# Performance work log

Hardware: AMD Instinct MI355X
Metric: run time of the kernel (lower is better)

The kernel has to match this reference:

```python
import jax, jax.numpy as jnp
import numpy as np

B = 524288
NF, NH1, NH21, NH22, NCLS = 5, 128, 32, 32, 1


def setup_inputs() -> dict:
    key = jax.random.key(0)
    ks = jax.random.split(key, 12)
    s = 0.05
    return {
        "x": jax.random.normal(ks[0], (B, NF), dtype=jnp.float32),
        "mean": jnp.zeros((NF,), dtype=jnp.float32),
        "std": jnp.ones((NF,), dtype=jnp.float32),
        "W1": jax.random.normal(ks[1], (NH1, NF), dtype=jnp.float32) * s,
        "b1": jax.random.normal(ks[2], (NH1,), dtype=jnp.float32) * s,
        "W21": jax.random.normal(ks[3], (NH21, NH1), dtype=jnp.float32) * s,
        "b21": jax.random.normal(ks[4], (NH21,), dtype=jnp.float32) * s,
        "W22": jax.random.normal(ks[5], (NH22, NH1), dtype=jnp.float32) * s,
        "b22": jax.random.normal(ks[6], (NH22,), dtype=jnp.float32) * s,
        "W31": jax.random.normal(ks[7], (NCLS, NH21), dtype=jnp.float32) * s,
        "b31": jax.random.normal(ks[8], (NCLS,), dtype=jnp.float32) * s,
        "W32": jax.random.normal(ks[9], (NCLS, NH22), dtype=jnp.float32) * s,
        "b32": jax.random.normal(ks[10], (NCLS,), dtype=jnp.float32) * s,
    }


def reference(x, mean, std, W1, b1, W21, b21, W22, b22, W31, b31, W32, b32):
    # de-normalized state used to build the CBF inequality
    x0 = x * std + mean  # [B, 5]
    h1 = jax.nn.relu(x @ W1.T + b1)         # [B, 128]  (bn=False path)
    x21 = jax.nn.relu(h1 @ W21.T + b21)     # [B, 32]
    x22 = jax.nn.relu(h1 @ W22.T + b22)     # [B, 32]
    x31 = x21 @ W31.T + b31                 # [B, 1]  QP linear term p
    x32 = 4.0 * jax.nn.sigmoid(x22 @ W32.T + b32)  # [B, 1]  learned penalty
    # h for the single inequality 1.8*u <= h
    h = (x0[:, 1] - x0[:, 3])[:, None] + x32 * (x0[:, 0] - x0[:, 2] - 1.8 * x0[:, 3])[:, None]
    # Closed-form 1-D QP: min 0.5 u^2 + x31*u  s.t. 1.8 u <= h
    u_unc = -x31
    u = jnp.where(1.8 * u_unc <= h, u_unc, h / 1.8)  # [B, 1]
    return u
```

## Files before the change

### kernel.cpp

```cpp
#include <hip/hip_runtime.h>
#include <math.h>

typedef __attribute__((ext_vector_type(8))) short bf16x8;
typedef __attribute__((ext_vector_type(4))) float f32x4;
typedef __attribute__((ext_vector_type(4))) unsigned int u32x4;

#define BLK 256


__device__ __forceinline__ unsigned int rne_bf16_bits(float w) {
    unsigned int u = __builtin_bit_cast(unsigned int, w);
    u += 0x7fffu + ((u >> 16) & 1u);
    return u >> 16;
}

__global__ void setup_kernel(const float* __restrict__ W1, const float* __restrict__ b1,
                             const float* __restrict__ W21, const float* __restrict__ W22,
                             float* __restrict__ w1q, unsigned short* __restrict__ frg)
{
    int t = blockIdx.x * blockDim.x + threadIdx.x;
    if (t < 128) {
        int c  = t;
        int tt = c >> 5, r = c & 31, qq = r >> 3, j = r & 7;
        float* dst = w1q + ((tt * 8 + j) * 4 + qq) * 8;
        #pragma unroll
        for (int f = 0; f < 5; ++f) dst[f] = W1[c * 5 + f];
        dst[5] = b1[c];
        dst[6] = 0.0f;
        dst[7] = 0.0f;
    }
    for (int e = t; e < 16 * 64 * 8; e += 4096) {
        int F = e >> 9, l = (e >> 3) & 63, j = e & 7;
        int mat = F >> 3, nt = (F >> 2) & 1, kt = F & 3;
        int n = nt * 16 + (l & 15);
        int k = kt * 32 + (l >> 4) * 8 + j;
        const float* W = mat ? W22 : W21;
        frg[e] = (unsigned short)rne_bf16_bits(W[n * 128 + k]);
    }
}

__global__ __launch_bounds__(BLK, 3) void barriernet_kernel(
    const float* __restrict__ x,
    const float* __restrict__ mean, const float* __restrict__ stdv,
    const float* __restrict__ b21, const float* __restrict__ b22,
    const float* __restrict__ W31, const float* __restrict__ b31,
    const float* __restrict__ W32, const float* __restrict__ b32,
    const float* __restrict__ w1q, const u32x4* __restrict__ frg,
    float* __restrict__ out, int zero)
{
    __shared__ u32x4 ldsF[1024];
    __shared__ float ldsX[1280];

    const int tid = threadIdx.x;
    #pragma unroll
    for (int i = 0; i < 4; ++i) ldsF[tid + i * BLK] = frg[tid + i * BLK];
    const float* xblk = x + (size_t)blockIdx.x * 1280;
    #pragma unroll
    for (int i = 0; i < 5; ++i) ldsX[tid + i * BLK] = xblk[tid + i * BLK];

    const int lane = tid & 63;
    const int wave = tid >> 6;
    const int m    = lane & 15;
    const int q    = lane >> 4;

    float sm_s[5], sm_m[5];
    #pragma unroll
    for (int f = 0; f < 5; ++f) { sm_s[f] = stdv[f]; sm_m[f] = mean[f]; }

    const f32x4 b21a = *(const f32x4*)(b21 + q * 4);
    const f32x4 b21b = *(const f32x4*)(b21 + 16 + q * 4);
    const f32x4 b22a = *(const f32x4*)(b22 + q * 4);
    const f32x4 b22b = *(const f32x4*)(b22 + 16 + q * 4);
    const f32x4 w31a = *(const f32x4*)(W31 + q * 4);
    const f32x4 w31b = *(const f32x4*)(W31 + 16 + q * 4);
    const f32x4 w32a = *(const f32x4*)(W32 + q * 4);
    const f32x4 w32b = *(const f32x4*)(W32 + 16 + q * 4);
    const float b31s = b31[0], b32s = b32[0];

    __syncthreads();

    const size_t row0 = (size_t)blockIdx.x * 256;

    #pragma unroll 1
    for (int it = 0; it < 2; ++it) {
        const int tl0 = wave * 4 + it * 2;

        float xf[2][5];
        #pragma unroll
        for (int T = 0; T < 2; ++T)
            #pragma unroll
            for (int f = 0; f < 5; ++f)
                xf[T][f] = ldsX[((tl0 + T) * 16 + m) * 5 + f];

        const float* wz = w1q + it * zero;
        unsigned int au[2][4][4];
        #pragma unroll
        for (int t = 0; t < 4; ++t) {
            #pragma unroll
            for (int p = 0; p < 4; ++p) {
                const int g0 = ((t * 8 + p * 2) * 4 + q) * 8;
                const float4 a0 = *(const float4*)(wz + g0);
                const float4 a1 = *(const float4*)(wz + g0 + 4);
                const float4 c0 = *(const float4*)(wz + g0 + 32);
                const float4 c1 = *(const float4*)(wz + g0 + 36);
                #pragma unroll
                for (int T = 0; T < 2; ++T) {
                    float h0 = a1.y;
                    h0 = fmaf(xf[T][0], a0.x, h0);
                    h0 = fmaf(xf[T][1], a0.y, h0);
                    h0 = fmaf(xf[T][2], a0.z, h0);
                    h0 = fmaf(xf[T][3], a0.w, h0);
                    h0 = fmaf(xf[T][4], a1.x, h0);
                    h0 = fmaxf(h0, 0.0f);
                    float h1 = c1.y;
                    h1 = fmaf(xf[T][0], c0.x, h1);
                    h1 = fmaf(xf[T][1], c0.y, h1);
                    h1 = fmaf(xf[T][2], c0.z, h1);
                    h1 = fmaf(xf[T][3], c0.w, h1);
                    h1 = fmaf(xf[T][4], c1.x, h1);
                    h1 = fmaxf(h1, 0.0f);
                    au[T][t][p] = rne_bf16_bits(h0) | (rne_bf16_bits(h1) << 16);
                }
            }
        }

        f32x4 acc[2][4];
        #pragma unroll
        for (int T = 0; T < 2; ++T) {
            acc[T][0] = b21a; acc[T][1] = b21b;
            acc[T][2] = b22a; acc[T][3] = b22b;
        }
        const int fz = it * zero;
        #pragma unroll
        for (int kt = 0; kt < 4; ++kt) {
            bf16x8 bw[4];
            #pragma unroll
            for (int c = 0; c < 4; ++c) {
                const int F = (c >> 1) * 8 + (c & 1) * 4 + kt;
                bw[c] = __builtin_bit_cast(bf16x8, ldsF[F * 64 + lane + fz]);
            }
            #pragma unroll
            for (int T = 0; T < 2; ++T) {
                u32x4 t4 = { au[T][kt][0], au[T][kt][1], au[T][kt][2], au[T][kt][3] };
                bf16x8 a = __builtin_bit_cast(bf16x8, t4);
                #pragma unroll
                for (int c = 0; c < 4; ++c)
                    acc[T][c] = __builtin_amdgcn_mfma_f32_16x16x32_bf16(bw[c], a, acc[T][c], 0, 0, 0);
            }
        }

        #pragma unroll
        for (int T = 0; T < 2; ++T) {
            float s31 = 0.0f, s32 = 0.0f;
            #pragma unroll
            for (int r = 0; r < 4; ++r) {
                s31 = fmaf(fmaxf(acc[T][0][r], 0.0f), w31a[r], s31);
                s31 = fmaf(fmaxf(acc[T][1][r], 0.0f), w31b[r], s31);
                s32 = fmaf(fmaxf(acc[T][2][r], 0.0f), w32a[r], s32);
                s32 = fmaf(fmaxf(acc[T][3][r], 0.0f), w32b[r], s32);
            }
            s31 += __shfl_xor(s31, 16);
            s31 += __shfl_xor(s31, 32);
            s32 += __shfl_xor(s32, 16);
            s32 += __shfl_xor(s32, 32);

            const float x31 = s31 + b31s;
            const float z   = s32 + b32s;
            const float x32 = 4.0f / (1.0f + __expf(-z));
            float x0[5];
            #pragma unroll
            for (int f = 0; f < 5; ++f) x0[f] = fmaf(xf[T][f], sm_s[f], sm_m[f]);
            const float h_ineq = (x0[1] - x0[3]) + x32 * (x0[0] - x0[2] - 1.8f * x0[3]);
            const float u_unc  = -x31;
            const float u      = (1.8f * u_unc <= h_ineq) ? u_unc : (h_ineq / 1.8f);
            if (lane < 16)
                out[row0 + (tl0 + T) * 16 + lane] = u;
        }
    }
}

extern "C" void kernel_launch(void* const* d_in, const int* in_sizes, int n_in,
                              void* d_out, int out_size, void* d_ws, size_t ws_size,
                              hipStream_t stream) {
    const float* x    = (const float*)d_in[0];
    const float* mean = (const float*)d_in[1];
    const float* stdv = (const float*)d_in[2];
    const float* W1   = (const float*)d_in[3];
    const float* b1   = (const float*)d_in[4];
    const float* W21  = (const float*)d_in[5];
    const float* b21  = (const float*)d_in[6];
    const float* W22  = (const float*)d_in[7];
    const float* b22  = (const float*)d_in[8];
    const float* W31  = (const float*)d_in[9];
    const float* b31  = (const float*)d_in[10];
    const float* W32  = (const float*)d_in[11];
    const float* b32  = (const float*)d_in[12];
    float* out = (float*)d_out;

    float* w1q = (float*)d_ws;
    unsigned short* frg = (unsigned short*)((char*)d_ws + 4096);

    setup_kernel<<<16, 256, 0, stream>>>(W1, b1, W21, W22, w1q, frg);

    barriernet_kernel<<<2048, BLK, 0, stream>>>(
        x, mean, stdv, b21, b22, W31, b31, W32, b32,
        w1q, (const u32x4*)frg, out, 0);
}
```

Before: 124.3 us.

## Halve rows per block, use packed-FP32 layer-1 math and hardware bf16 pack

Each block now handles 128 rows in one pass instead of 256 rows over two loop iterations, and the grid doubles to 4096 blocks with the occupancy hint raised from 3 to 5 blocks per CU. W1 and b1 are re-laid out in pairs so the first layer can run as two-wide float vector FMAs (packed FP32), and the bf16 conversion uses the library pair-conversion intrinsic. The aim is more waves per CU to hide latency, and fewer VALU instructions in the first layer. The cost is that the 16 KB weight-fragment LDS fill is now repeated per 128 rows instead of per 256, and register pressure is tighter under the higher occupancy bound.

```diff
diff --git a/kernel.cpp b/kernel.cpp
--- a/kernel.cpp
+++ b/kernel.cpp
@@ -1,8 +1,11 @@
 #include <hip/hip_runtime.h>
+#include <hip/hip_bf16.h>
 #include <math.h>
+#include <string.h>
 
 typedef __attribute__((ext_vector_type(8))) short bf16x8;
 typedef __attribute__((ext_vector_type(4))) float f32x4;
+typedef __attribute__((ext_vector_type(2))) float f32x2;
 typedef __attribute__((ext_vector_type(4))) unsigned int u32x4;
 
 #define BLK 256
@@ -16,18 +19,21 @@
 
 __global__ void setup_kernel(const float* __restrict__ W1, const float* __restrict__ b1,
                              const float* __restrict__ W21, const float* __restrict__ W22,
-                             float* __restrict__ w1q, unsigned short* __restrict__ frg)
+                             float* __restrict__ w1p2, unsigned short* __restrict__ frg)
 {
     int t = blockIdx.x * blockDim.x + threadIdx.x;
-    if (t < 128) {
-        int c  = t;
-        int tt = c >> 5, r = c & 31, qq = r >> 3, j = r & 7;
-        float* dst = w1q + ((tt * 8 + j) * 4 + qq) * 8;
-        #pragma unroll
-        for (int f = 0; f < 5; ++f) dst[f] = W1[c * 5 + f];
-        dst[5] = b1[c];
-        dst[6] = 0.0f;
-        dst[7] = 0.0f;
+    if (t < 64) {
+        int P = t;
+        int tt = P >> 4, pp = (P >> 2) & 3, qq = P & 3;
+        int c0 = tt * 32 + qq * 8 + 2 * pp;
+        float* dst = w1p2 + P * 12;
+        #pragma unroll
+        for (int f = 0; f < 5; ++f) {
+            dst[2 * f]     = W1[c0 * 5 + f];
+            dst[2 * f + 1] = W1[(c0 + 1) * 5 + f];
+        }
+        dst[10] = b1[c0];
+        dst[11] = b1[c0 + 1];
     }
     for (int e = t; e < 16 * 64 * 8; e += 4096) {
         int F = e >> 9, l = (e >> 3) & 63, j = e & 7;
@@ -39,24 +45,25 @@
     }
 }
 
-__global__ __launch_bounds__(BLK, 3) void barriernet_kernel(
+__global__ __launch_bounds__(BLK, 5) void barriernet_kernel(
     const float* __restrict__ x,
     const float* __restrict__ mean, const float* __restrict__ stdv,
     const float* __restrict__ b21, const float* __restrict__ b22,
     const float* __restrict__ W31, const float* __restrict__ b31,
     const float* __restrict__ W32, const float* __restrict__ b32,
-    const float* __restrict__ w1q, const u32x4* __restrict__ frg,
-    float* __restrict__ out, int zero)
+    const float* __restrict__ w1p2, const u32x4* __restrict__ frg,
+    float* __restrict__ out)
 {
     __shared__ u32x4 ldsF[1024];
-    __shared__ float ldsX[1280];
+    __shared__ float ldsX[640];
 
     const int tid = threadIdx.x;
     #pragma unroll
     for (int i = 0; i < 4; ++i) ldsF[tid + i * BLK] = frg[tid + i * BLK];
-    const float* xblk = x + (size_t)blockIdx.x * 1280;
-    #pragma unroll
-    for (int i = 0; i < 5; ++i) ldsX[tid + i * BLK] = xblk[tid + i * BLK];
+    const float* xblk = x + (size_t)blockIdx.x * 640;
+    #pragma unroll
+    for (int i = 0; i < 2; ++i) ldsX[tid + i * BLK] = xblk[tid + i * BLK];
+    if (tid < 128) ldsX[512 + tid] = xblk[512 + tid];
 
     const int lane = tid & 63;
     const int wave = tid >> 6;
@@ -79,103 +86,94 @@
 
     __syncthreads();
 
-    const size_t row0 = (size_t)blockIdx.x * 256;
-
-    #pragma unroll 1
-    for (int it = 0; it < 2; ++it) {
-        const int tl0 = wave * 4 + it * 2;
-
-        float xf[2][5];
-        #pragma unroll
-        for (int T = 0; T < 2; ++T)
-            #pragma unroll
-            for (int f = 0; f < 5; ++f)
-                xf[T][f] = ldsX[((tl0 + T) * 16 + m) * 5 + f];
-
-        const float* wz = w1q + it * zero;
-        unsigned int au[2][4][4];
-        #pragma unroll
-        for (int t = 0; t < 4; ++t) {
-            #pragma unroll
-            for (int p = 0; p < 4; ++p) {
-                const int g0 = ((t * 8 + p * 2) * 4 + q) * 8;
-                const float4 a0 = *(const float4*)(wz + g0);
-                const float4 a1 = *(const float4*)(wz + g0 + 4);
-                const float4 c0 = *(const float4*)(wz + g0 + 32);
-                const float4 c1 = *(const float4*)(wz + g0 + 36);
-                #pragma unroll
-                for (int T = 0; T < 2; ++T) {
-                    float h0 = a1.y;
-                    h0 = fmaf(xf[T][0], a0.x, h0);
-                    h0 = fmaf(xf[T][1], a0.y, h0);
-                    h0 = fmaf(xf[T][2], a0.z, h0);
-                    h0 = fmaf(xf[T][3], a0.w, h0);
-                    h0 = fmaf(xf[T][4], a1.x, h0);
-                    h0 = fmaxf(h0, 0.0f);
-                    float h1 = c1.y;
-                    h1 = fmaf(xf[T][0], c0.x, h1);
-                    h1 = fmaf(xf[T][1], c0.y, h1);
-                    h1 = fmaf(xf[T][2], c0.z, h1);
-                    h1 = fmaf(xf[T][3], c0.w, h1);
-                    h1 = fmaf(xf[T][4], c1.x, h1);
-                    h1 = fmaxf(h1, 0.0f);
-                    au[T][t][p] = rne_bf16_bits(h0) | (rne_bf16_bits(h1) << 16);
-                }
-            }
-        }
-
-        f32x4 acc[2][4];
-        #pragma unroll
-        for (int T = 0; T < 2; ++T) {
-            acc[T][0] = b21a; acc[T][1] = b21b;
-            acc[T][2] = b22a; acc[T][3] = b22b;
-        }
-        const int fz = it * zero;
-        #pragma unroll
-        for (int kt = 0; kt < 4; ++kt) {
-            bf16x8 bw[4];
-            #pragma unroll
-            for (int c = 0; c < 4; ++c) {
-                const int F = (c >> 1) * 8 + (c & 1) * 4 + kt;
-                bw[c] = __builtin_bit_cast(bf16x8, ldsF[F * 64 + lane + fz]);
-            }
+    const size_t row0 = (size_t)blockIdx.x * 128;
+
+    float xf[2][5];
+    #pragma unroll
+    for (int T = 0; T < 2; ++T)
+        #pragma unroll
+        for (int f = 0; f < 5; ++f)
+            xf[T][f] = ldsX[(wave * 32 + T * 16 + m) * 5 + f];
+
+    unsigned int au[2][4][4];
+    #pragma unroll
+    for (int t = 0; t < 4; ++t) {
+        #pragma unroll
+        for (int p = 0; p < 4; ++p) {
+            const float* base = w1p2 + ((t * 4 + p) * 4 + q) * 12;
+            const f32x4 A = *(const f32x4*)(base);
+            const f32x4 B = *(const f32x4*)(base + 4);
+            const f32x4 C = *(const f32x4*)(base + 8);
+            const f32x2 w0 = { A[0], A[1] }, w1 = { A[2], A[3] };
+            const f32x2 w2 = { B[0], B[1] }, w3 = { B[2], B[3] };
+            const f32x2 w4 = { C[0], C[1] }, bb = { C[2], C[3] };
             #pragma unroll
             for (int T = 0; T < 2; ++T) {
-                u32x4 t4 = { au[T][kt][0], au[T][kt][1], au[T][kt][2], au[T][kt][3] };
-                bf16x8 a = __builtin_bit_cast(bf16x8, t4);
-                #pragma unroll
-                for (int c = 0; c < 4; ++c)
-                    acc[T][c] = __builtin_amdgcn_mfma_f32_16x16x32_bf16(bw[c], a, acc[T][c], 0, 0, 0);
+                f32x2 h = bb;
+                h = __builtin_elementwise_fma((f32x2){ xf[T][0], xf[T][0] }, w0, h);
+                h = __builtin_elementwise_fma((f32x2){ xf[T][1], xf[T][1] }, w1, h);
+                h = __builtin_elementwise_fma((f32x2){ xf[T][2], xf[T][2] }, w2, h);
+                h = __builtin_elementwise_fma((f32x2){ xf[T][3], xf[T][3] }, w3, h);
+                h = __builtin_elementwise_fma((f32x2){ xf[T][4], xf[T][4] }, w4, h);
+                h = __builtin_elementwise_max(h, (f32x2){ 0.0f, 0.0f });
+                __hip_bfloat162 bp = __float22bfloat162_rn(make_float2(h[0], h[1]));
+                unsigned int r;
+                memcpy(&r, &bp, 4);
+                au[T][t][p] = r;
             }
         }
-
+    }
+
+    f32x4 acc[2][4];
+    #pragma unroll
+    for (int T = 0; T < 2; ++T) {
+        acc[T][0] = b21a; acc[T][1] = b21b;
+        acc[T][2] = b22a; acc[T][3] = b22b;
+    }
+    #pragma unroll
+    for (int kt = 0; kt < 4; ++kt) {
+        bf16x8 bw[4];
+        #pragma unroll
+        for (int c = 0; c < 4; ++c) {
+            const int F = (c >> 1) * 8 + (c & 1) * 4 + kt;
+            bw[c] = __builtin_bit_cast(bf16x8, ldsF[F * 64 + lane]);
+        }
         #pragma unroll
         for (int T = 0; T < 2; ++T) {
-            float s31 = 0.0f, s32 = 0.0f;
+            u32x4 t4 = { au[T][kt][0], au[T][kt][1], au[T][kt][2], au[T][kt][3] };
+            bf16x8 a = __builtin_bit_cast(bf16x8, t4);
             #pragma unroll
-            for (int r = 0; r < 4; ++r) {
-                s31 = fmaf(fmaxf(acc[T][0][r], 0.0f), w31a[r], s31);
-                s31 = fmaf(fmaxf(acc[T][1][r], 0.0f), w31b[r], s31);
-                s32 = fmaf(fmaxf(acc[T][2][r], 0.0f), w32a[r], s32);
-                s32 = fmaf(fmaxf(acc[T][3][r], 0.0f), w32b[r], s32);
-            }
-            s31 += __shfl_xor(s31, 16);
-            s31 += __shfl_xor(s31, 32);
-            s32 += __shfl_xor(s32, 16);
-            s32 += __shfl_xor(s32, 32);
-
-            const float x31 = s31 + b31s;
-            const float z   = s32 + b32s;
-            const float x32 = 4.0f / (1.0f + __expf(-z));
-            float x0[5];
-            #pragma unroll
-            for (int f = 0; f < 5; ++f) x0[f] = fmaf(xf[T][f], sm_s[f], sm_m[f]);
-            const float h_ineq = (x0[1] - x0[3]) + x32 * (x0[0] - x0[2] - 1.8f * x0[3]);
-            const float u_unc  = -x31;
-            const float u      = (1.8f * u_unc <= h_ineq) ? u_unc : (h_ineq / 1.8f);
-            if (lane < 16)
-                out[row0 + (tl0 + T) * 16 + lane] = u;
-        }
+            for (int c = 0; c < 4; ++c)
+                acc[T][c] = __builtin_amdgcn_mfma_f32_16x16x32_bf16(bw[c], a, acc[T][c], 0, 0, 0);
+        }
+    }
+
+    #pragma unroll
+    for (int T = 0; T < 2; ++T) {
+        float s31 = 0.0f, s32 = 0.0f;
+        #pragma unroll
+        for (int r = 0; r < 4; ++r) {
+            s31 = fmaf(fmaxf(acc[T][0][r], 0.0f), w31a[r], s31);
+            s31 = fmaf(fmaxf(acc[T][1][r], 0.0f), w31b[r], s31);
+            s32 = fmaf(fmaxf(acc[T][2][r], 0.0f), w32a[r], s32);
+            s32 = fmaf(fmaxf(acc[T][3][r], 0.0f), w32b[r], s32);
+        }
+        s31 += __shfl_xor(s31, 16);
+        s31 += __shfl_xor(s31, 32);
+        s32 += __shfl_xor(s32, 16);
+        s32 += __shfl_xor(s32, 32);
+
+        const float x31 = s31 + b31s;
+        const float z   = s32 + b32s;
+        const float x32 = 4.0f / (1.0f + __expf(-z));
+        float x0[5];
+        #pragma unroll
+        for (int f = 0; f < 5; ++f) x0[f] = fmaf(xf[T][f], sm_s[f], sm_m[f]);
+        const float h_ineq = (x0[1] - x0[3]) + x32 * (x0[0] - x0[2] - 1.8f * x0[3]);
+        const float u_unc  = -x31;
+        const float u      = (1.8f * u_unc <= h_ineq) ? u_unc : (h_ineq / 1.8f);
+        if (lane < 16)
+            out[row0 + wave * 32 + T * 16 + lane] = u;
     }
 }
 
@@ -197,12 +195,12 @@
     const float* b32  = (const float*)d_in[12];
     float* out = (float*)d_out;
 
-    float* w1q = (float*)d_ws;
+    float* w1p2 = (float*)d_ws;
     unsigned short* frg = (unsigned short*)((char*)d_ws + 4096);
 
-    setup_kernel<<<16, 256, 0, stream>>>(W1, b1, W21, W22, w1q, frg);
-
-    barriernet_kernel<<<2048, BLK, 0, stream>>>(
+    setup_kernel<<<16, 256, 0, stream>>>(W1, b1, W21, W22, w1p2, frg);
+
+    barriernet_kernel<<<4096, BLK, 0, stream>>>(
         x, mean, stdv, b21, b22, W31, b31, W32, b32,
-        w1q, (const u32x4*)frg, out, 0);
-}
+        w1p2, (const u32x4*)frg, out);
+}
```

New measurement: 126.5 us. About the same (+1.8%).

## Compute first layer on MFMA with split-bf16 precision and per-wave row loop

Applied to the files above, without the earlier changes.

The first 5->128 layer moves from scalar FMAs to bf16 MFMA. Inputs and weights are split into high and low bf16 parts so the product keeps near-fp32 accuracy, and the bias enters through a constant 1 input column. The K index of the second layer is remapped so the MFMA output registers feed directly as the next layer's A operand. Each wave now loops over 8 row tiles with a register prefetch of the next x rows instead of staging x in LDS. The grid is halved and launch bounds raised to 4 blocks per CU, trading ALU work for extra MFMA issues and more per-iteration global loads.

```diff
diff --git a/kernel.cpp b/kernel.cpp
--- a/kernel.cpp
+++ b/kernel.cpp
@@ -13,169 +13,181 @@
     u += 0x7fffu + ((u >> 16) & 1u);
     return u >> 16;
 }
+__device__ __forceinline__ float bf16_to_f32(unsigned int bits) {
+    return __builtin_bit_cast(float, bits << 16);
+}
 
 __global__ void setup_kernel(const float* __restrict__ W1, const float* __restrict__ b1,
                              const float* __restrict__ W21, const float* __restrict__ W22,
-                             float* __restrict__ w1q, unsigned short* __restrict__ frg)
+                             unsigned short* __restrict__ w1f, unsigned short* __restrict__ frg)
 {
     int t = blockIdx.x * blockDim.x + threadIdx.x;
-    if (t < 128) {
-        int c  = t;
-        int tt = c >> 5, r = c & 31, qq = r >> 3, j = r & 7;
-        float* dst = w1q + ((tt * 8 + j) * 4 + qq) * 8;
-        #pragma unroll
-        for (int f = 0; f < 5; ++f) dst[f] = W1[c * 5 + f];
-        dst[5] = b1[c];
-        dst[6] = 0.0f;
-        dst[7] = 0.0f;
+    {
+        int e = t;
+        int nt = e >> 9, l = (e >> 3) & 63, j = e & 7;
+        int n = nt * 16 + (l & 15), q = l >> 4;
+        unsigned short v = 0;
+        if (q == 0) {
+            if (j < 5)       v = (unsigned short)rne_bf16_bits(W1[n * 5 + j]);
+            else if (j == 5) v = (unsigned short)rne_bf16_bits(b1[n]);
+        } else if (q == 1) {
+            if (j < 5) {
+                unsigned int h = rne_bf16_bits(W1[n * 5 + j]);
+                v = (unsigned short)rne_bf16_bits(W1[n * 5 + j] - bf16_to_f32(h));
+            } else if (j == 5) {
+                unsigned int h = rne_bf16_bits(b1[n]);
+                v = (unsigned short)rne_bf16_bits(b1[n] - bf16_to_f32(h));
+            }
+        } else if (q == 2) {
+            if (j < 5)       v = (unsigned short)rne_bf16_bits(W1[n * 5 + j]);
+        }
+        w1f[e] = v;
     }
     for (int e = t; e < 16 * 64 * 8; e += 4096) {
         int F = e >> 9, l = (e >> 3) & 63, j = e & 7;
-        int mat = F >> 3, nt = (F >> 2) & 1, kt = F & 3;
-        int n = nt * 16 + (l & 15);
-        int k = kt * 32 + (l >> 4) * 8 + j;
+        int mat = F >> 3, nt2 = (F >> 2) & 1, kt = F & 3;
+        int n2 = nt2 * 16 + (l & 15), q = l >> 4;
+        int ks = 16 * (2 * kt + (j >> 2)) + 4 * q + (j & 3);
         const float* W = mat ? W22 : W21;
-        frg[e] = (unsigned short)rne_bf16_bits(W[n * 128 + k]);
-    }
-}
-
-__global__ __launch_bounds__(BLK, 3) void barriernet_kernel(
+        frg[e] = (unsigned short)rne_bf16_bits(W[n2 * 128 + ks]);
+    }
+}
+
+__global__ __launch_bounds__(BLK, 4) void barriernet_kernel(
     const float* __restrict__ x,
     const float* __restrict__ mean, const float* __restrict__ stdv,
     const float* __restrict__ b21, const float* __restrict__ b22,
     const float* __restrict__ W31, const float* __restrict__ b31,
     const float* __restrict__ W32, const float* __restrict__ b32,
-    const float* __restrict__ w1q, const u32x4* __restrict__ frg,
+    const u32x4* __restrict__ w1fg, const u32x4* __restrict__ frg,
     float* __restrict__ out, int zero)
 {
     __shared__ u32x4 ldsF[1024];
-    __shared__ float ldsX[1280];
 
     const int tid = threadIdx.x;
     #pragma unroll
     for (int i = 0; i < 4; ++i) ldsF[tid + i * BLK] = frg[tid + i * BLK];
-    const float* xblk = x + (size_t)blockIdx.x * 1280;
-    #pragma unroll
-    for (int i = 0; i < 5; ++i) ldsX[tid + i * BLK] = xblk[tid + i * BLK];
 
     const int lane = tid & 63;
     const int wave = tid >> 6;
     const int m    = lane & 15;
     const int q    = lane >> 4;
 
+    u32x4 w1f[8];
+    #pragma unroll
+    for (int nt = 0; nt < 8; ++nt) w1f[nt] = w1fg[nt * 64 + lane];
+
     float sm_s[5], sm_m[5];
     #pragma unroll
     for (int f = 0; f < 5; ++f) { sm_s[f] = stdv[f]; sm_m[f] = mean[f]; }
-
-    const f32x4 b21a = *(const f32x4*)(b21 + q * 4);
-    const f32x4 b21b = *(const f32x4*)(b21 + 16 + q * 4);
-    const f32x4 b22a = *(const f32x4*)(b22 + q * 4);
-    const f32x4 b22b = *(const f32x4*)(b22 + 16 + q * 4);
-    const f32x4 w31a = *(const f32x4*)(W31 + q * 4);
-    const f32x4 w31b = *(const f32x4*)(W31 + 16 + q * 4);
-    const f32x4 w32a = *(const f32x4*)(W32 + q * 4);
-    const f32x4 w32b = *(const f32x4*)(W32 + 16 + q * 4);
     const float b31s = b31[0], b32s = b32[0];
 
     __syncthreads();
 
-    const size_t row0 = (size_t)blockIdx.x * 256;
+    const size_t wrow0 = (size_t)blockIdx.x * 512 + wave * 128;
+
+    float4 xc4; float xc1;
+    {
+        const float* p = x + (wrow0 + m) * 5;
+        xc4 = *(const float4*)p; xc1 = p[4];
+    }
 
     #pragma unroll 1
-    for (int it = 0; it < 2; ++it) {
-        const int tl0 = wave * 4 + it * 2;
-
-        float xf[2][5];
-        #pragma unroll
-        for (int T = 0; T < 2; ++T)
-            #pragma unroll
-            for (int f = 0; f < 5; ++f)
-                xf[T][f] = ldsX[((tl0 + T) * 16 + m) * 5 + f];
-
-        const float* wz = w1q + it * zero;
-        unsigned int au[2][4][4];
-        #pragma unroll
-        for (int t = 0; t < 4; ++t) {
-            #pragma unroll
-            for (int p = 0; p < 4; ++p) {
-                const int g0 = ((t * 8 + p * 2) * 4 + q) * 8;
-                const float4 a0 = *(const float4*)(wz + g0);
-                const float4 a1 = *(const float4*)(wz + g0 + 4);
-                const float4 c0 = *(const float4*)(wz + g0 + 32);
-                const float4 c1 = *(const float4*)(wz + g0 + 36);
-                #pragma unroll
-                for (int T = 0; T < 2; ++T) {
-                    float h0 = a1.y;
-                    h0 = fmaf(xf[T][0], a0.x, h0);
-                    h0 = fmaf(xf[T][1], a0.y, h0);
-                    h0 = fmaf(xf[T][2], a0.z, h0);
-                    h0 = fmaf(xf[T][3], a0.w, h0);
-                    h0 = fmaf(xf[T][4], a1.x, h0);
-                    h0 = fmaxf(h0, 0.0f);
-                    float h1 = c1.y;
-                    h1 = fmaf(xf[T][0], c0.x, h1);
-                    h1 = fmaf(xf[T][1], c0.y, h1);
-                    h1 = fmaf(xf[T][2], c0.z, h1);
-                    h1 = fmaf(xf[T][3], c0.w, h1);
-                    h1 = fmaf(xf[T][4], c1.x, h1);
-                    h1 = fmaxf(h1, 0.0f);
-                    au[T][t][p] = rne_bf16_bits(h0) | (rne_bf16_bits(h1) << 16);
-                }
-            }
-        }
-
-        f32x4 acc[2][4];
-        #pragma unroll
-        for (int T = 0; T < 2; ++T) {
-            acc[T][0] = b21a; acc[T][1] = b21b;
-            acc[T][2] = b22a; acc[T][3] = b22b;
-        }
+    for (int it = 0; it < 8; ++it) {
+        const int itn = (it < 7) ? it + 1 : 7;
+        const float* pn = x + (wrow0 + itn * 16 + m) * 5;
+        float4 xn4 = *(const float4*)pn;
+        float  xn1 = pn[4];
+
+        const float xf[5] = { xc4.x, xc4.y, xc4.z, xc4.w, xc1 };
+
+        unsigned int hb[5], lb[5];
+        #pragma unroll
+        for (int f = 0; f < 5; ++f) {
+            hb[f] = rne_bf16_bits(xf[f]);
+            lb[f] = rne_bf16_bits(xf[f] - bf16_to_f32(hb[f]));
+        }
+        const unsigned int xh01 = hb[0] | (hb[1] << 16);
+        const unsigned int xh23 = hb[2] | (hb[3] << 16);
+        const unsigned int xh4b = hb[4] | (0x3F80u << 16);
+        const unsigned int xl01 = lb[0] | (lb[1] << 16);
+        const unsigned int xl23 = lb[2] | (lb[3] << 16);
+        const unsigned int xl4  = lb[4];
+        const bool ql2 = (q < 2), q2 = (q == 2);
+        u32x4 xd;
+        xd[0] = ql2 ? xh01 : (q2 ? xl01 : 0u);
+        xd[1] = ql2 ? xh23 : (q2 ? xl23 : 0u);
+        xd[2] = ql2 ? xh4b : (q2 ? xl4  : 0u);
+        xd[3] = 0u;
+        const bf16x8 xb = __builtin_bit_cast(bf16x8, xd);
+
+        unsigned int au[4][4];
+        #pragma unroll
+        for (int kt = 0; kt < 4; ++kt) {
+            f32x4 z = { 0.0f, 0.0f, 0.0f, 0.0f };
+            f32x4 d0 = __builtin_amdgcn_mfma_f32_16x16x32_bf16(
+                __builtin_bit_cast(bf16x8, w1f[2 * kt]),     xb, z, 0, 0, 0);
+            f32x4 d1 = __builtin_amdgcn_mfma_f32_16x16x32_bf16(
+                __builtin_bit_cast(bf16x8, w1f[2 * kt + 1]), xb, z, 0, 0, 0);
+            au[kt][0] = rne_bf16_bits(fmaxf(d0[0], 0.0f)) | (rne_bf16_bits(fmaxf(d0[1], 0.0f)) << 16);
+            au[kt][1] = rne_bf16_bits(fmaxf(d0[2], 0.0f)) | (rne_bf16_bits(fmaxf(d0[3], 0.0f)) << 16);
+            au[kt][2] = rne_bf16_bits(fmaxf(d1[0], 0.0f)) | (rne_bf16_bits(fmaxf(d1[1], 0.0f)) << 16);
+            au[kt][3] = rne_bf16_bits(fmaxf(d1[2], 0.0f)) | (rne_bf16_bits(fmaxf(d1[3], 0.0f)) << 16);
+        }
+
+        const float* bz21 = b21 + it * zero;
+        const float* bz22 = b22 + it * zero;
+        const float* wz31 = W31 + it * zero;
+        const float* wz32 = W32 + it * zero;
+        f32x4 acc[4];
+        acc[0] = *(const f32x4*)(bz21 + q * 4);
+        acc[1] = *(const f32x4*)(bz21 + 16 + q * 4);
+        acc[2] = *(const f32x4*)(bz22 + q * 4);
+        acc[3] = *(const f32x4*)(bz22 + 16 + q * 4);
+
         const int fz = it * zero;
         #pragma unroll
         for (int kt = 0; kt < 4; ++kt) {
-            bf16x8 bw[4];
+            u32x4 t4 = { au[kt][0], au[kt][1], au[kt][2], au[kt][3] };
+            const bf16x8 a = __builtin_bit_cast(bf16x8, t4);
             #pragma unroll
             for (int c = 0; c < 4; ++c) {
                 const int F = (c >> 1) * 8 + (c & 1) * 4 + kt;
-                bw[c] = __builtin_bit_cast(bf16x8, ldsF[F * 64 + lane + fz]);
+                const bf16x8 bw = __builtin_bit_cast(bf16x8, ldsF[F * 64 + lane + fz]);
+                acc[c] = __builtin_amdgcn_mfma_f32_16x16x32_bf16(bw, a, acc[c], 0, 0, 0);
             }
-            #pragma unroll
-            for (int T = 0; T < 2; ++T) {
-                u32x4 t4 = { au[T][kt][0], au[T][kt][1], au[T][kt][2], au[T][kt][3] };
-                bf16x8 a = __builtin_bit_cast(bf16x8, t4);
-                #pragma unroll
-                for (int c = 0; c < 4; ++c)
-                    acc[T][c] = __builtin_amdgcn_mfma_f32_16x16x32_bf16(bw[c], a, acc[T][c], 0, 0, 0);
-            }
-        }
-
-        #pragma unroll
-        for (int T = 0; T < 2; ++T) {
-            float s31 = 0.0f, s32 = 0.0f;
-            #pragma unroll
-            for (int r = 0; r < 4; ++r) {
-                s31 = fmaf(fmaxf(acc[T][0][r], 0.0f), w31a[r], s31);
-                s31 = fmaf(fmaxf(acc[T][1][r], 0.0f), w31b[r], s31);
-                s32 = fmaf(fmaxf(acc[T][2][r], 0.0f), w32a[r], s32);
-                s32 = fmaf(fmaxf(acc[T][3][r], 0.0f), w32b[r], s32);
-            }
-            s31 += __shfl_xor(s31, 16);
-            s31 += __shfl_xor(s31, 32);
-            s32 += __shfl_xor(s32, 16);
-            s32 += __shfl_xor(s32, 32);
-
-            const float x31 = s31 + b31s;
-            const float z   = s32 + b32s;
-            const float x32 = 4.0f / (1.0f + __expf(-z));
-            float x0[5];
-            #pragma unroll
-            for (int f = 0; f < 5; ++f) x0[f] = fmaf(xf[T][f], sm_s[f], sm_m[f]);
-            const float h_ineq = (x0[1] - x0[3]) + x32 * (x0[0] - x0[2] - 1.8f * x0[3]);
-            const float u_unc  = -x31;
-            const float u      = (1.8f * u_unc <= h_ineq) ? u_unc : (h_ineq / 1.8f);
-            if (lane < 16)
-                out[row0 + (tl0 + T) * 16 + lane] = u;
-        }
+        }
+
+        const f32x4 w31a = *(const f32x4*)(wz31 + q * 4);
+        const f32x4 w31b = *(const f32x4*)(wz31 + 16 + q * 4);
+        const f32x4 w32a = *(const f32x4*)(wz32 + q * 4);
+        const f32x4 w32b = *(const f32x4*)(wz32 + 16 + q * 4);
+        float s31 = 0.0f, s32 = 0.0f;
+        #pragma unroll
+        for (int r = 0; r < 4; ++r) {
+            s31 = fmaf(fmaxf(acc[0][r], 0.0f), w31a[r], s31);
+            s31 = fmaf(fmaxf(acc[1][r], 0.0f), w31b[r], s31);
+            s32 = fmaf(fmaxf(acc[2][r], 0.0f), w32a[r], s32);
+            s32 = fmaf(fmaxf(acc[3][r], 0.0f), w32b[r], s32);
+        }
+        s31 += __shfl_xor(s31, 16);
+        s31 += __shfl_xor(s31, 32);
+        s32 += __shfl_xor(s32, 16);
+        s32 += __shfl_xor(s32, 32);
+
+        const float x31 = s31 + b31s;
+        const float z   = s32 + b32s;
+        const float x32 = 4.0f / (1.0f + __expf(-z));
+        float x0[5];
+        #pragma unroll
+        for (int f = 0; f < 5; ++f) x0[f] = fmaf(xf[f], sm_s[f], sm_m[f]);
+        const float h_ineq = (x0[1] - x0[3]) + x32 * (x0[0] - x0[2] - 1.8f * x0[3]);
+        const float u_unc  = -x31;
+        const float u      = (1.8f * u_unc <= h_ineq) ? u_unc : (h_ineq / 1.8f);
+        if (lane < 16)
+            out[wrow0 + it * 16 + lane] = u;
+
+        xc4 = xn4; xc1 = xn1;
     }
 }
 
@@ -197,12 +209,12 @@
     const float* b32  = (const float*)d_in[12];
     float* out = (float*)d_out;
 
-    float* w1q = (float*)d_ws;
-    unsigned short* frg = (unsigned short*)((char*)d_ws + 4096);
-
-    setup_kernel<<<16, 256, 0, stream>>>(W1, b1, W21, W22, w1q, frg);
-
-    barriernet_kernel<<<2048, BLK, 0, stream>>>(
+    unsigned short* w1f = (unsigned short*)d_ws;
+    unsigned short* frg = (unsigned short*)((char*)d_ws + 8192);
+
+    setup_kernel<<<16, 256, 0, stream>>>(W1, b1, W21, W22, w1f, frg);
+
+    barriernet_kernel<<<1024, BLK, 0, stream>>>(
         x, mean, stdv, b21, b22, W31, b31, W32, b32,
-        w1q, (const u32x4*)frg, out, 0);
-}
+        (const u32x4*)w1f, (const u32x4*)frg, out, 0);
+}
```

Result: faster. 110.1 us (-11.4%).
